# Kernel tuning notes

Hardware: AMD Instinct MI355X
Metric: run time of the kernel (lower is better)

The kernel has to match this reference:

```python
import jax, jax.numpy as jnp
import numpy as np

VOLUME_RES = np.array([1.0, 1.0, 1.0], dtype=np.float32)
OUTPUT_SHAPE = (256, 256, 256)
NOISE_STD = 0.01
DOWNSAMPLE_THRESHOLD = 1.1


def setup_inputs() -> dict:
    key = jax.random.key(0)
    k1, k2 = jax.random.split(key)
    B, C, D, H, W = 2, 1, 256, 256, 256
    image = jax.random.normal(k1, (B, C, D, H, W), dtype=jnp.float32)
    acquisition_res = jnp.tile(jnp.array([1, 1, 4], dtype=jnp.int32), (B, 1))
    # pre-generated Gaussian noise (already scaled by noise_std), output-shaped
    noise = jax.random.normal(k2, (B, C) + OUTPUT_SHAPE, dtype=jnp.float32) * NOISE_STD
    return {"image": image, "acquisition_res": acquisition_res, "noise": noise}


def _nearest_resize(x, out_shape):
    # torch F.interpolate mode='nearest': src_idx = floor(dst_idx * in / out)
    for ax, (insz, outsz) in enumerate(zip(x.shape[2:], out_shape)):
        if insz != outsz:
            idx = (jnp.arange(outsz) * insz // outsz).astype(jnp.int32)
            x = jnp.take(x, idx, axis=ax + 2)
    return x


def reference(image, acquisition_res, noise):
    # All batch rows share the same acquisition_res, so the per-sample torch
    # loop collapses to one vectorized batched 3D FFT (same math per sample).
    acq = np.asarray(acquisition_res)[0].astype(np.float32)
    factors = acq / VOLUME_RES
    axis = int(np.argmax(factors))          # spatial axis to crop (0=D,1=H,2=W)
    factor = float(factors[axis])
    spatial_axes = (2, 3, 4)

    x = image
    if factor > DOWNSAMPLE_THRESHOLD:
        f = jnp.fft.fftshift(jnp.fft.fftn(x, axes=spatial_axes), axes=spatial_axes)
        ax = axis + 2
        n = x.shape[ax]
        new_size = int(round(n / factor))
        start = n // 2 - new_size // 2      # centered k-space crop
        f = jax.lax.slice_in_dim(f, start, start + new_size, axis=ax)
        x = jnp.fft.ifftn(jnp.fft.ifftshift(f, axes=spatial_axes), axes=spatial_axes).real
        if x.shape[2:] != OUTPUT_SHAPE:
            x = _nearest_resize(x, OUTPUT_SHAPE)
    # prob_noise = 1.0 -> noise always added; noise is pre-scaled by noise_std
    return x + noise
```

## Files before the change

### kernel.cpp

```cpp
#include <hip/hip_runtime.h>
#include <hip/hip_bf16.h>
#include <math.h>


typedef __attribute__((ext_vector_type(8))) short short8;
typedef __attribute__((ext_vector_type(4))) float floatx4;

__device__ __forceinline__ short f2bf(float f) {
    __hip_bfloat16 h = __float2bfloat16(f);
    return *reinterpret_cast<short*>(&h);
}

__global__ void gen_b_kernel(short* __restrict__ Bg) {
    int i = blockIdx.x * 256 + threadIdx.x;
    int j    = i & 7;
    int lane = (i >> 3) & 63;
    int st   = i >> 9;
    int t = st & 3, s = st >> 2;
    int k = s * 32 + (lane >> 4) * 8 + j;
    int n = t * 16 + (lane & 15);
    int tt = (4 * n - k) & 255;
    double g;
    if (tt == 0) {
        g = 1.0;
    } else {
        double th = M_PI * (double)tt / 256.0;
        g = (sin(63.0 * th) / sin(th) + cos(64.0 * th)) * (1.0 / 64.0);
    }
    Bg[i] = f2bf((float)g);
}

__global__ __launch_bounds__(256, 4) void fdds_kernel(
    const float* __restrict__ img, const float* __restrict__ noise,
    const short* __restrict__ Bg, float* __restrict__ out) {
    __shared__ short8 Bs[2048];
    const int tid = threadIdx.x;
#pragma unroll
    for (int i = 0; i < 8; ++i) {
        const int idx = tid + 256 * i;
        Bs[idx] = *(const short8*)(Bg + idx * 8);
    }
    __syncthreads();

    const int lane = tid & 63;
    const int wave = tid >> 6;
    const int mrow = lane & 15;
    const int kgrp = lane >> 4;

    const int line0 = (blockIdx.x * 4 + wave) * 16;
    const float* ap = img + (line0 + mrow) * 256 + kgrp * 8;

    floatx4 acc[4];
#pragma unroll
    for (int t = 0; t < 4; ++t) acc[t] = (floatx4)0.0f;

#pragma unroll
    for (int s = 0; s < 8; ++s) {
        floatx4 a0 = *(const floatx4*)(ap + s * 32);
        floatx4 a1 = *(const floatx4*)(ap + s * 32 + 4);
        short8 af;
        af[0] = f2bf(a0[0]); af[1] = f2bf(a0[1]);
        af[2] = f2bf(a0[2]); af[3] = f2bf(a0[3]);
        af[4] = f2bf(a1[0]); af[5] = f2bf(a1[1]);
        af[6] = f2bf(a1[2]); af[7] = f2bf(a1[3]);
#pragma unroll
        for (int t = 0; t < 4; ++t)
            acc[t] = __builtin_amdgcn_mfma_f32_16x16x32_bf16(
                af, Bs[(s * 4 + t) * 64 + lane], acc[t], 0, 0, 0);
    }

#pragma unroll
    for (int r = 0; r < 4; ++r) {
        const int line = line0 + kgrp * 4 + r;
        const float* np = noise + line * 256;
        float* op = out + line * 256;
#pragma unroll
        for (int t = 0; t < 4; ++t) {
            const int n = t * 16 + mrow;
            floatx4 nz = *(const floatx4*)(np + 4 * n);
            floatx4 o = nz + acc[t][r];
            __builtin_nontemporal_store(o, (floatx4*)(op + 4 * n));
        }
    }
}

extern "C" void kernel_launch(void* const* d_in, const int* in_sizes, int n_in,
                              void* d_out, int out_size, void* d_ws, size_t ws_size,
                              hipStream_t stream) {
    const float* img   = (const float*)d_in[0];
    const float* noise = (const float*)d_in[2];
    float* out = (float*)d_out;
    short* Bg = (short*)d_ws;

    gen_b_kernel<<<64, 256, 0, stream>>>(Bg);
    fdds_kernel<<<2048, 256, 0, stream>>>(img, noise, Bg, out);
}
```

Before: 331.1 us.

## Process two row tiles per wave with early image loads and batched noise loads

Each wave now handles two 16-line tiles, which halves the grid and amortizes the per-block LDS fill of the B matrix. The image loads for the first tile are issued before the LDS fill, and the second tile's loads are issued right after the first tile's MFMAs. This overlaps global-load latency with the LDS fill, the compute and the epilogue. Noise loads are grouped eight at a time before the stores. The costs are more registers, which is why occupancy is lowered to 3 blocks in the launch bounds, and fewer blocks to hide memory latency.

New measurement: 329.9 us. Within noise of the previous version (-0.4%).

```diff
diff --git a/kernel.cpp b/kernel.cpp
--- a/kernel.cpp
+++ b/kernel.cpp
@@ -30,11 +30,24 @@
     Bg[i] = f2bf((float)g);
 }
 
-__global__ __launch_bounds__(256, 4) void fdds_kernel(
+__global__ __launch_bounds__(256, 3) void fdds_kernel(
     const float* __restrict__ img, const float* __restrict__ noise,
     const short* __restrict__ Bg, float* __restrict__ out) {
     __shared__ short8 Bs[2048];
-    const int tid = threadIdx.x;
+    const int tid  = threadIdx.x;
+    const int lane = tid & 63;
+    const int wave = tid >> 6;
+    const int mrow = lane & 15;
+    const int kgrp = lane >> 4;
+
+    const int line0 = blockIdx.x * 128 + wave * 32;
+    const float* ap = img + (line0 + mrow) * 256 + kgrp * 8;
+
+    floatx4 a[16];
+#pragma unroll
+    for (int i = 0; i < 16; ++i)
+        a[i] = *(const floatx4*)(ap + (i >> 1) * 32 + (i & 1) * 4);
+
 #pragma unroll
     for (int i = 0; i < 8; ++i) {
         const int idx = tid + 256 * i;
@@ -42,44 +55,48 @@
     }
     __syncthreads();
 
-    const int lane = tid & 63;
-    const int wave = tid >> 6;
-    const int mrow = lane & 15;
-    const int kgrp = lane >> 4;
-
-    const int line0 = (blockIdx.x * 4 + wave) * 16;
-    const float* ap = img + (line0 + mrow) * 256 + kgrp * 8;
-
-    floatx4 acc[4];
 #pragma unroll
-    for (int t = 0; t < 4; ++t) acc[t] = (floatx4)0.0f;
+    for (int tile = 0; tile < 2; ++tile) {
+        floatx4 acc[4];
+#pragma unroll
+        for (int t = 0; t < 4; ++t) acc[t] = (floatx4)0.0f;
 
 #pragma unroll
-    for (int s = 0; s < 8; ++s) {
-        floatx4 a0 = *(const floatx4*)(ap + s * 32);
-        floatx4 a1 = *(const floatx4*)(ap + s * 32 + 4);
-        short8 af;
-        af[0] = f2bf(a0[0]); af[1] = f2bf(a0[1]);
-        af[2] = f2bf(a0[2]); af[3] = f2bf(a0[3]);
-        af[4] = f2bf(a1[0]); af[5] = f2bf(a1[1]);
-        af[6] = f2bf(a1[2]); af[7] = f2bf(a1[3]);
+        for (int s = 0; s < 8; ++s) {
+            short8 af;
+            af[0] = f2bf(a[2 * s][0]); af[1] = f2bf(a[2 * s][1]);
+            af[2] = f2bf(a[2 * s][2]); af[3] = f2bf(a[2 * s][3]);
+            af[4] = f2bf(a[2 * s + 1][0]); af[5] = f2bf(a[2 * s + 1][1]);
+            af[6] = f2bf(a[2 * s + 1][2]); af[7] = f2bf(a[2 * s + 1][3]);
 #pragma unroll
-        for (int t = 0; t < 4; ++t)
-            acc[t] = __builtin_amdgcn_mfma_f32_16x16x32_bf16(
-                af, Bs[(s * 4 + t) * 64 + lane], acc[t], 0, 0, 0);
-    }
+            for (int t = 0; t < 4; ++t)
+                acc[t] = __builtin_amdgcn_mfma_f32_16x16x32_bf16(
+                    af, Bs[(s * 4 + t) * 64 + lane], acc[t], 0, 0, 0);
+        }
 
+        if (tile == 0) {
+            const float* ap1 = ap + 16 * 256;
 #pragma unroll
-    for (int r = 0; r < 4; ++r) {
-        const int line = line0 + kgrp * 4 + r;
-        const float* np = noise + line * 256;
-        float* op = out + line * 256;
+            for (int i = 0; i < 16; ++i)
+                a[i] = *(const floatx4*)(ap1 + (i >> 1) * 32 + (i & 1) * 4);
+        }
+
+        const int lineb = line0 + tile * 16 + kgrp * 4;
 #pragma unroll
-        for (int t = 0; t < 4; ++t) {
-            const int n = t * 16 + mrow;
-            floatx4 nz = *(const floatx4*)(np + 4 * n);
-            floatx4 o = nz + acc[t][r];
-            __builtin_nontemporal_store(o, (floatx4*)(op + 4 * n));
+        for (int rp = 0; rp < 2; ++rp) {
+            floatx4 nz[8];
+#pragma unroll
+            for (int i = 0; i < 8; ++i) {
+                const int r = rp * 2 + (i >> 2), t = i & 3;
+                nz[i] = *(const floatx4*)(noise + (lineb + r) * 256 + 4 * (t * 16 + mrow));
+            }
+#pragma unroll
+            for (int i = 0; i < 8; ++i) {
+                const int r = rp * 2 + (i >> 2), t = i & 3;
+                floatx4 o = nz[i] + acc[t][r];
+                __builtin_nontemporal_store(
+                    o, (floatx4*)(out + (lineb + r) * 256 + 4 * (t * 16 + mrow)));
+            }
         }
     }
 }
@@ -93,5 +110,5 @@
     short* Bg = (short*)d_ws;
 
     gen_b_kernel<<<64, 256, 0, stream>>>(Bg);
-    fdds_kernel<<<2048, 256, 0, stream>>>(img, noise, Bg, out);
+    fdds_kernel<<<1024, 256, 0, stream>>>(img, noise, Bg, out);
 }
```

## Double-buffer image tiles into LDS via async global_load_lds with manual waitcnts

Applied to the files above, without the earlier changes.

Each block now processes four 16-line tiles per wave instead of one. The image rows are streamed into a per-wave double-buffered LDS area with global_load_lds while MFMAs run on the previous chunk. Noise is prefetched into registers ahead of the epilogue, and explicit vmcnt/lgkmcnt waits and sched barriers control the overlap. The grid shrinks to a quarter and occupancy drops to 2 blocks per SIMD. The goal is to hide HBM latency and amortise the per-block load of the B matrix into LDS, at the cost of more LDS and register pressure and fragile hand-written counter waits.

After: 328.3 us. No clear change (-0.8%).

```diff
diff --git a/kernel.cpp b/kernel.cpp
--- a/kernel.cpp
+++ b/kernel.cpp
@@ -30,11 +30,36 @@
     Bg[i] = f2bf((float)g);
 }
 
-__global__ __launch_bounds__(256, 4) void fdds_kernel(
+typedef __attribute__((address_space(1))) const void gas_void;
+typedef __attribute__((address_space(3))) void las_void;
+
+__device__ __forceinline__ void stage4(const float* g, float* l) {
+#pragma unroll
+    for (int i = 0; i < 4; ++i)
+        __builtin_amdgcn_global_load_lds((gas_void*)(g + i * 1024),
+                                         (las_void*)(l + i * 256), 16, 0, 0);
+}
+
+#define SCHED_FENCE() __builtin_amdgcn_sched_barrier(0)
+
+__global__ __launch_bounds__(256, 2) void fdds_kernel(
     const float* __restrict__ img, const float* __restrict__ noise,
     const short* __restrict__ Bg, float* __restrict__ out) {
     __shared__ short8 Bs[2048];
-    const int tid = threadIdx.x;
+    __shared__ __align__(16) float Abuf[4][2][1024];
+
+    const int tid  = threadIdx.x;
+    const int lane = tid & 63;
+    const int wave = tid >> 6;
+    const int mrow = lane & 15;
+    const int kgrp = lane >> 4;
+
+    const long lineW = (long)blockIdx.x * 256 + wave * 64;
+    const float* gA = img + lineW * 256 + (lane >> 4) * 256 + (lane & 15) * 4;
+
+    stage4(gA + 0,  &Abuf[wave][0][0]);
+    stage4(gA + 64, &Abuf[wave][1][0]);
+
 #pragma unroll
     for (int i = 0; i < 8; ++i) {
         const int idx = tid + 256 * i;
@@ -42,44 +67,68 @@
     }
     __syncthreads();
 
-    const int lane = tid & 63;
-    const int wave = tid >> 6;
-    const int mrow = lane & 15;
-    const int kgrp = lane >> 4;
-
-    const int line0 = (blockIdx.x * 4 + wave) * 16;
-    const float* ap = img + (line0 + mrow) * 256 + kgrp * 8;
-
     floatx4 acc[4];
 #pragma unroll
     for (int t = 0; t < 4; ++t) acc[t] = (floatx4)0.0f;
+    floatx4 nz[16];
 
 #pragma unroll
-    for (int s = 0; s < 8; ++s) {
-        floatx4 a0 = *(const floatx4*)(ap + s * 32);
-        floatx4 a1 = *(const floatx4*)(ap + s * 32 + 4);
-        short8 af;
-        af[0] = f2bf(a0[0]); af[1] = f2bf(a0[1]);
-        af[2] = f2bf(a0[2]); af[3] = f2bf(a0[3]);
-        af[4] = f2bf(a1[0]); af[5] = f2bf(a1[1]);
-        af[6] = f2bf(a1[2]); af[7] = f2bf(a1[3]);
+    for (int j = 0; j < 16; ++j) {
+        const int p   = j & 3;
+        const int tau = j >> 2;
+
+        if (p == 0) {
+            const long lineb = lineW + tau * 16 + kgrp * 4;
 #pragma unroll
-        for (int t = 0; t < 4; ++t)
-            acc[t] = __builtin_amdgcn_mfma_f32_16x16x32_bf16(
-                af, Bs[(s * 4 + t) * 64 + lane], acc[t], 0, 0, 0);
-    }
+            for (int i = 0; i < 16; ++i) {
+                const int r = i >> 2, t = i & 3;
+                nz[i] = *(const floatx4*)(noise + (lineb + r) * 256 + 4 * (t * 16 + mrow));
+            }
+            SCHED_FENCE();
+        }
 
+        if (j == 15)               { asm volatile("s_waitcnt vmcnt(0)"  ::: "memory"); }
+        else if (p == 0 || p == 1) { if (j >= 4) asm volatile("s_waitcnt vmcnt(36)" ::: "memory"); }
+        else if (j >= 2)           { asm volatile("s_waitcnt vmcnt(4)"  ::: "memory"); }
+        SCHED_FENCE();
+
+        const float* ab = &Abuf[wave][j & 1][0] + mrow * 64 + kgrp * 8;
 #pragma unroll
-    for (int r = 0; r < 4; ++r) {
-        const int line = line0 + kgrp * 4 + r;
-        const float* np = noise + line * 256;
-        float* op = out + line * 256;
+        for (int ks = 0; ks < 2; ++ks) {
+            floatx4 a0 = *(const floatx4*)(ab + ks * 32);
+            floatx4 a1 = *(const floatx4*)(ab + ks * 32 + 4);
+            short8 af;
+            af[0] = f2bf(a0[0]); af[1] = f2bf(a0[1]);
+            af[2] = f2bf(a0[2]); af[3] = f2bf(a0[3]);
+            af[4] = f2bf(a1[0]); af[5] = f2bf(a1[1]);
+            af[6] = f2bf(a1[2]); af[7] = f2bf(a1[3]);
+            const int s = p * 2 + ks;
 #pragma unroll
-        for (int t = 0; t < 4; ++t) {
-            const int n = t * 16 + mrow;
-            floatx4 nz = *(const floatx4*)(np + 4 * n);
-            floatx4 o = nz + acc[t][r];
-            __builtin_nontemporal_store(o, (floatx4*)(op + 4 * n));
+            for (int t = 0; t < 4; ++t)
+                acc[t] = __builtin_amdgcn_mfma_f32_16x16x32_bf16(
+                    af, Bs[(s * 4 + t) * 64 + lane], acc[t], 0, 0, 0);
+        }
+
+        asm volatile("s_waitcnt lgkmcnt(0)" ::: "memory");
+        SCHED_FENCE();
+        if (j + 2 < 16) {
+            const int jn = j + 2;
+            stage4(gA + (jn >> 2) * 4096 + (jn & 3) * 64, &Abuf[wave][jn & 1][0]);
+        }
+        SCHED_FENCE();
+
+        if (p == 3) {
+            const long lineb = lineW + tau * 16 + kgrp * 4;
+#pragma unroll
+            for (int i = 0; i < 16; ++i) {
+                const int r = i >> 2, t = i & 3;
+                floatx4 o = nz[i] + acc[t][r];
+                __builtin_nontemporal_store(
+                    o, (floatx4*)(out + (lineb + r) * 256 + 4 * (t * 16 + mrow)));
+            }
+#pragma unroll
+            for (int t = 0; t < 4; ++t) acc[t] = (floatx4)0.0f;
+            SCHED_FENCE();
         }
     }
 }
@@ -93,5 +142,5 @@
     short* Bg = (short*)d_ws;
 
     gen_b_kernel<<<64, 256, 0, stream>>>(Bg);
-    fdds_kernel<<<2048, 256, 0, stream>>>(img, noise, Bg, out);
+    fdds_kernel<<<512, 256, 0, stream>>>(img, noise, Bg, out);
 }
```
